# Kernel optimization log

Measured on AMD Instinct MI355X. Metric: run time of the kernel, lower is better.

The kernel has to match this reference:

```python
import jax, jax.numpy as jnp
import numpy as np

N_CLASSES = 4
N_STEPS = 10
THRESHOLD = 0.7
ALPHA = 2.0


def _make_kernel_bias(n_classes, threshold):
    cross = np.zeros((3, 3, 3), dtype=np.float32)
    cross[1, 1, :] = 1.0
    cross[1, :, 1] = 1.0
    cross[:, 1, 1] = 1.0
    # depthwise kernel, OIDHW with I = 1 (groups = n_classes)
    kernel = (1.0 / 7.0 / (1.0 - threshold)) * np.tile(cross[None, None], (n_classes, 1, 1, 1, 1))
    bias = np.full((n_classes,), -threshold / (1.0 - threshold), dtype=np.float32)
    return jnp.asarray(kernel), jnp.asarray(bias)


def setup_inputs() -> dict:
    key = jax.random.key(0)
    k1, k2, k3 = jax.random.split(key, 3)
    B, C, D, H, W = 2, N_CLASSES, 128, 128, 128
    inp = jax.random.normal(k1, (B, C, D, H, W), dtype=jnp.float32)
    target = jax.random.randint(k2, (B, D, H, W), 0, C, dtype=jnp.int64)
    weight = jax.random.uniform(k3, (B, C), dtype=jnp.float32)
    kernel, bias = _make_kernel_bias(C, THRESHOLD)
    return {"input": inp, "target": target, "weight": weight, "kernel": kernel, "bias": bias}


def _erode(op, kernel, bias, n_classes):
    y = jax.lax.conv_general_dilated(
        op, kernel, window_strides=(1, 1, 1), padding=[(1, 1)] * 3,
        dimension_numbers=("NCDHW", "OIDHW", "NCDHW"),
        feature_group_count=n_classes)
    return jnp.maximum(y + bias[None, :, None, None, None], 0.0)


def reference(input, target, weight, kernel, bias):
    C = N_CLASSES
    probs = jax.nn.softmax(input, axis=1)
    # one_hot -> [B, D, H, W, C] -> [B, C, D, H, W]
    tgt = jnp.transpose(jax.nn.one_hot(target, C, dtype=probs.dtype), (0, 4, 1, 2, 3))
    op = jnp.square(probs - tgt)
    loss_t = jnp.zeros_like(op)
    for k in range(N_STEPS):
        op = _erode(op, kernel, bias, C)
        loss_t = loss_t + (float(k + 1) ** ALPHA) * op
    loss_t = loss_t * weight[:, :, None, None, None]
    return jnp.mean(loss_t)
```

## Files before the change

kernel.cpp:

```cpp
#include <hip/hip_runtime.h>

#define DHW   (128*128*128)
#define CDHW  (4*DHW)
#define NTOT  (2*CDHW)
#define NACC  1024

#define ROW4     32
#define IN_ROWS  12
#define S1_ROWS  10
#define IN_P4    (IN_ROWS*ROW4)
#define S1_P4    (S1_ROWS*ROW4)
#define SLOT4(z) (((z)+8)&3)
#define SLOT2(z) (((z)+8)&1)


__global__ __launch_bounds__(256, 4) void fused_sm_erode2_kernel(
    const float* __restrict__ in, const int* __restrict__ tgt,
    float4* __restrict__ dst,
    const float* __restrict__ kern, const float* __restrict__ bias,
    const float* __restrict__ weight, float c1, float c2,
    double* __restrict__ accs, int* __restrict__ flagOut)
{
    __shared__ float4 lin[4 * IN_P4];
    __shared__ float4 ls1[2 * S1_P4];
    __shared__ double wsum[4];
    __shared__ int    voteArr[16];

    const int tid = threadIdx.x;
    const int x  = blockIdx.x & 7;
    const int q  = blockIdx.x >> 3;
    const int c  = q & 3;
    const int t  = x * 32 + (q >> 2);
    const int y0 = (t & 15) << 3;
    const int zb = ((t >> 4) & 7) << 4;
    const int b  = (t >> 7) & 1;
    const int bc = b * 4 + c;
    const int fid = (bc << 7) | (((t >> 4) & 7) << 4) | (t & 15);

    const float4* in4 = (const float4*)in;
    const int4*   tg4 = (const int4*)tgt;
    const size_t  chb = ((size_t)(b * 4)) << 19;
    const size_t  co0 = chb + ((size_t)c << 19);
    const size_t  co1 = chb + ((size_t)((c + 1) & 3) << 19);
    const size_t  co2 = chb + ((size_t)((c + 2) & 3) << 19);
    const size_t  co3 = chb + ((size_t)((c + 3) & 3) << 19);
    float4*       dp  = dst + ((size_t)bc << 19);
    const float wk = kern[13];
    const float bs = bias[c];

    const int col  = tid & 31;
    const int trow = tid >> 5;

    if (tid < 16) voteArr[tid] = 0;

    const int  gy0  = y0 + trow - 2;
    const bool lv0  = ((unsigned)gy0 < 128u);
    const int  off0 = (lv0 ? gy0 : 0) * 32 + col;
    const bool act1 = (tid < 128);
    const int  gy1  = y0 + trow + 6;
    const bool lv1  = act1 && ((unsigned)gy1 < 128u);
    const int  off1 = (lv1 ? gy1 : 0) * 32 + col;

    const bool  sact1 = (tid < 64);
    const int   sr  = (tid < 32) ? 0 : 9;
    const float m1  = ((unsigned)(y0 + sr - 1) < 128u) ? 1.f : 0.f;
    const int   ci1 = (sr + 1) * 32 + (tid & 31);
    const int   so1 = sr * 32 + (tid & 31);

    const float lmask = (col == 0)  ? 0.f : 1.f;
    const float rmask = (col == 31) ? 0.f : 1.f;

    const int go4 = (y0 + trow) * 32 + col;

    const float4 f4z = make_float4(0.f, 0.f, 0.f, 0.f);
    float4 A00 = f4z, A01 = f4z, A02 = f4z, A03 = f4z;
    float4 A10 = f4z, A11 = f4z, A12 = f4z, A13 = f4z;
    int4   T0 = make_int4(0,0,0,0), T1 = make_int4(0,0,0,0);
    bool   ok0 = false, ok1 = false;
    float4 s_m = f4z, s_c = f4z, s_p = f4z;
    float4 vH  = f4z;

    auto prefetch = [&](int L) {
        const bool zok = ((unsigned)L < 128u);
        ok0 = zok && lv0;
        ok1 = zok && lv1;
        if (ok0) {
            size_t o = (size_t)(L << 12) + off0;
            A00 = in4[co0 + o];
            A01 = in4[co1 + o];
            A02 = in4[co2 + o];
            A03 = in4[co3 + o];
            T0  = tg4[((size_t)b << 19) + o];
        }
        if (ok1) {
            size_t o = (size_t)(L << 12) + off1;
            A10 = in4[co0 + o];
            A11 = in4[co1 + o];
            A12 = in4[co2 + o];
            A13 = in4[co3 + o];
            T1  = tg4[((size_t)b << 19) + o];
        }
    };
    auto op_one = [&](const float4& B0, const float4& B1, const float4& B2,
                      const float4& B3, const int4& T) -> float4 {
        float4 r;
        #define OP1(K)                                                         \
        {                                                                      \
            float vc = B0.K;                                                   \
            float sm = 1.0f + __expf(B1.K - vc) + __expf(B2.K - vc)            \
                            + __expf(B3.K - vc);                               \
            float d  = __builtin_amdgcn_rcpf(sm) - ((T.K == c) ? 1.0f : 0.0f); \
            r.K = d * d;                                                       \
        }
        OP1(x) OP1(y) OP1(z) OP1(w)
        #undef OP1
        return r;
    };
    auto commit = [&](int L) {
        float4* sl = lin + SLOT4(L) * IN_P4;
        float4 v0 = f4z, v1 = f4z;
        if (ok0) v0 = op_one(A00, A01, A02, A03, T0);
        if (ok1) v1 = op_one(A10, A11, A12, A13, T1);
        sl[tid] = v0;
        if (act1) sl[256 + tid] = v1;
    };
    auto s1one = [&](const float4* pzm, const float4* pzc, const float4* pzp,
                     int ci, float ym) -> float4 {
        float4 qC = pzc[ci];
        float4 qU = pzc[ci - 32];
        float4 qD = pzc[ci + 32];
        float4 qm = pzm[ci];
        float4 qp = pzp[ci];
        float lf = __shfl_up(qC.w, 1, 64)   * lmask;
        float rt = __shfl_down(qC.x, 1, 64) * rmask;
        float4 v;
        v.x = fmaxf((qC.x + lf   + qC.y + qU.x + qD.x + qm.x + qp.x) * wk + bs, 0.f) * ym;
        v.y = fmaxf((qC.y + qC.x + qC.z + qU.y + qD.y + qm.y + qp.y) * wk + bs, 0.f) * ym;
        v.z = fmaxf((qC.z + qC.y + qC.w + qU.z + qD.z + qm.z + qp.z) * wk + bs, 0.f) * ym;
        v.w = fmaxf((qC.w + qC.z + rt   + qU.w + qD.w + qm.w + qp.w) * wk + bs, 0.f) * ym;
        return v;
    };
    auto s1_phase = [&](int z) {
        float4* o = ls1 + SLOT2(z) * S1_P4;
        float4 vnew;
        if ((unsigned)z < 128u) {
            const float4* pzm = lin + SLOT4(z - 1) * IN_P4;
            const float4* pzc = lin + SLOT4(z)     * IN_P4;
            const float4* pzp = lin + SLOT4(z + 1) * IN_P4;
            vnew = s1one(pzm, pzc, pzp, tid + 64, 1.f);
            o[tid + 32] = vnew;
            if (sact1) o[so1] = s1one(pzm, pzc, pzp, ci1, m1);
        } else {
            vnew = f4z;
            o[tid + 32] = f4z;
            if (sact1) o[so1] = f4z;
        }
        s_m = s_c; s_c = s_p; s_p = vnew;
    };

    double part = 0.0;

    prefetch(zb - 2); commit(zb - 2);
    prefetch(zb - 1); commit(zb - 1);
    prefetch(zb);     commit(zb);
    prefetch(zb + 1);
    __syncthreads();
    s1_phase(zb - 1);

    for (int L = zb + 1; L <= zb + 17; ++L) {
        commit(L);
        __syncthreads();
        const int zp = L - 3;
        if (zp >= zb && voteArr[zp - zb] != 0)
            dp[((size_t)zp << 12) + go4] = vH;
        if (L <= zb + 16) prefetch(L + 1);
        s1_phase(L - 1);
        const int zo = L - 2;
        if (zo >= zb) {
            const float4* su = ls1 + SLOT2(zo) * S1_P4;
            float4 u4 = su[tid];
            float4 d4 = su[tid + 64];
            float lf = __shfl_up(s_c.w, 1, 64)   * lmask;
            float rt = __shfl_down(s_c.x, 1, 64) * rmask;
            float4 v;
            v.x = fmaxf((s_c.x + lf    + s_c.y + u4.x + d4.x + s_m.x + s_p.x) * wk + bs, 0.f);
            v.y = fmaxf((s_c.y + s_c.x + s_c.z + u4.y + d4.y + s_m.y + s_p.y) * wk + bs, 0.f);
            v.z = fmaxf((s_c.z + s_c.y + s_c.w + u4.z + d4.z + s_m.z + s_p.z) * wk + bs, 0.f);
            v.w = fmaxf((s_c.w + s_c.z + rt    + u4.w + d4.w + s_m.w + s_p.w) * wk + bs, 0.f);
            float pl = c1 * (s_c.x + s_c.y + s_c.z + s_c.w)
                     + c2 * (v.x   + v.y   + v.z   + v.w);
            part += (double)pl;
            bool nzv = (v.x != 0.f) || (v.y != 0.f) || (v.z != 0.f) || (v.w != 0.f);
            if (__any(nzv) && (tid & 63) == 0) atomicOr(&voteArr[zo - zb], 1);
            vH = v;
        }
    }

    __syncthreads();
    if (voteArr[15] != 0) dp[((size_t)(zb + 15) << 12) + go4] = vH;

    #pragma unroll
    for (int off = 32; off > 0; off >>= 1)
        part += __shfl_down(part, off, 64);
    if ((tid & 63) == 0) wsum[tid >> 6] = part;
    __syncthreads();
    if (tid == 0) {
        int mask = 0;
        #pragma unroll
        for (int i = 0; i < 16; ++i) mask |= (voteArr[i] ? 1 : 0) << i;
        flagOut[fid] = mask;
        double tot = (wsum[0] + wsum[1] + wsum[2] + wsum[3]) * (double)weight[bc];
        accs[blockIdx.x] = tot;
    }
}

__global__ __launch_bounds__(256, 4) void erode2_kernel(
    const float4* __restrict__ src, float4* __restrict__ dst,
    const float* __restrict__ kern, const float* __restrict__ bias,
    const float* __restrict__ weight, float c1, float c2,
    int store, double* __restrict__ accs,
    const int* __restrict__ flagIn, int* __restrict__ flagOut)
{
    __shared__ float4 lin[4 * IN_P4];
    __shared__ float4 ls1[2 * S1_P4];
    __shared__ double wsum[4];
    __shared__ int    sf[9];
    __shared__ int    voteArr[16];

    const int tid = threadIdx.x;
    const int bid = ((blockIdx.x & 7) << 7) | (blockIdx.x >> 3);
    const int ty = bid & 15;
    const int tz = (bid >> 4) & 7;
    const int y0 = ty << 3;
    const int zb = tz << 4;
    const int bc = bid >> 7;

    if (tid < 9) {
        int dy = tid % 3 - 1, dz = tid / 3 - 1;
        int yt = ty + dy, zt = tz + dz;
        int f = 0;
        if ((unsigned)yt < 16u && (unsigned)zt < 8u)
            f = flagIn[(bc << 7) | (zt << 4) | yt];
        sf[tid] = f;
    }
    if (tid < 16) voteArr[tid] = 0;
    __syncthreads();

    unsigned aInW = 0;
    #pragma unroll
    for (int i = 0; i < 20; ++i) {
        int L = zb - 2 + i;
        if ((unsigned)L < 128u) {
            int zi = (L >> 4) - tz + 1;
            int m  = sf[zi * 3] | sf[zi * 3 + 1] | sf[zi * 3 + 2];
            aInW |= (unsigned)((m >> (L & 15)) & 1) << i;
        }
    }
    if (aInW == 0) {
        if (tid == 0) flagOut[bid] = 0;
        return;
    }
    const unsigned aS1W = aInW | (aInW << 1) | (aInW >> 1);
    const unsigned aS2W = aS1W | (aS1W << 1) | (aS1W >> 1);

    const float4* sp = src + ((size_t)bc << 19);
    float4*       dp = dst + ((size_t)bc << 19);
    const float wk = kern[13];
    const float bs = bias[bc & 3];

    const int col  = tid & 31;
    const int trow = tid >> 5;

    const int  gy0  = y0 + trow - 2;
    const bool lv0  = ((unsigned)gy0 < 128u);
    const int  off0 = (lv0 ? gy0 : 0) * 32 + col;
    const bool act1 = (tid < 128);
    const int  gy1  = y0 + trow + 6;
    const bool lv1  = act1 && ((unsigned)gy1 < 128u);
    const int  off1 = (lv1 ? gy1 : 0) * 32 + col;

    const int yd0c = (unsigned)((gy0 >> 3) - ty + 1) < 3u ? ((gy0 >> 3) - ty + 1) : 1;
    const int yd1c = (unsigned)((gy1 >> 3) - ty + 1) < 3u ? ((gy1 >> 3) - ty + 1) : 1;

    const bool  sact1 = (tid < 64);
    const int   sr  = (tid < 32) ? 0 : 9;
    const float m1  = ((unsigned)(y0 + sr - 1) < 128u) ? 1.f : 0.f;
    const int   ci1 = (sr + 1) * 32 + (tid & 31);
    const int   so1 = sr * 32 + (tid & 31);

    const float lmask = (col == 0)  ? 0.f : 1.f;
    const float rmask = (col == 31) ? 0.f : 1.f;

    const int go4 = (y0 + trow) * 32 + col;

    const float4 f4z = make_float4(0.f, 0.f, 0.f, 0.f);
    float4 pf0 = f4z, pf1 = f4z;
    float4 s_m = f4z, s_c = f4z, s_p = f4z;
    float4 vH  = f4z;

    auto prefetch = [&](int L) {
        pf0 = f4z; pf1 = f4z;
        if ((unsigned)L < 128u) {
            const int zi = (L >> 4) - tz + 1;
            const int sh = L & 15;
            const float4* zp = sp + ((size_t)L << 12);
            if (lv0 && ((sf[zi * 3 + yd0c] >> sh) & 1)) pf0 = zp[off0];
            if (lv1 && ((sf[zi * 3 + yd1c] >> sh) & 1)) pf1 = zp[off1];
        }
    };
    auto commit = [&](int L) {
        float4* sl = lin + SLOT4(L) * IN_P4;
        sl[tid] = pf0;
        if (act1) sl[256 + tid] = pf1;
    };
    auto s1one = [&](const float4* pzm, const float4* pzc, const float4* pzp,
                     int ci, float ym) -> float4 {
        float4 qC = pzc[ci];
        float4 qU = pzc[ci - 32];
        float4 qD = pzc[ci + 32];
        float4 qm = pzm[ci];
        float4 qp = pzp[ci];
        float lf = __shfl_up(qC.w, 1, 64)   * lmask;
        float rt = __shfl_down(qC.x, 1, 64) * rmask;
        float4 v;
        v.x = fmaxf((qC.x + lf   + qC.y + qU.x + qD.x + qm.x + qp.x) * wk + bs, 0.f) * ym;
        v.y = fmaxf((qC.y + qC.x + qC.z + qU.y + qD.y + qm.y + qp.y) * wk + bs, 0.f) * ym;
        v.z = fmaxf((qC.z + qC.y + qC.w + qU.z + qD.z + qm.z + qp.z) * wk + bs, 0.f) * ym;
        v.w = fmaxf((qC.w + qC.z + rt   + qU.w + qD.w + qm.w + qp.w) * wk + bs, 0.f) * ym;
        return v;
    };
    auto s1_phase = [&](int z) {
        float4 vnew = f4z;
        if ((unsigned)z < 128u && ((aS1W >> (z - zb + 2)) & 1)) {
            float4* o = ls1 + SLOT2(z) * S1_P4;
            const float4* pzm = lin + SLOT4(z - 1) * IN_P4;
            const float4* pzc = lin + SLOT4(z)     * IN_P4;
            const float4* pzp = lin + SLOT4(z + 1) * IN_P4;
            vnew = s1one(pzm, pzc, pzp, tid + 64, 1.f);
            o[tid + 32] = vnew;
            if (sact1) o[so1] = s1one(pzm, pzc, pzp, ci1, m1);
        }
        s_m = s_c; s_c = s_p; s_p = vnew;
    };

    double part = 0.0;

    prefetch(zb - 2); commit(zb - 2);
    prefetch(zb - 1); commit(zb - 1);
    prefetch(zb);     commit(zb);
    prefetch(zb + 1);
    __syncthreads();
    s1_phase(zb - 1);

    for (int L = zb + 1; L <= zb + 17; ++L) {
        commit(L);
        __syncthreads();
        const int zp = L - 3;
        if (store && zp >= zb && voteArr[zp - zb] != 0)
            dp[((size_t)zp << 12) + go4] = vH;
        if (L <= zb + 16) prefetch(L + 1);
        s1_phase(L - 1);
        const int zo = L - 2;
        if (zo >= zb) {
            float4 v = f4z;
            if ((aS2W >> (zo - zb + 2)) & 1) {
                float4 u4 = f4z, d4 = f4z;
                if ((aS1W >> (zo - zb + 2)) & 1) {
                    const float4* su = ls1 + SLOT2(zo) * S1_P4;
                    u4 = su[tid];
                    d4 = su[tid + 64];
                }
                float lf = __shfl_up(s_c.w, 1, 64)   * lmask;
                float rt = __shfl_down(s_c.x, 1, 64) * rmask;
                v.x = fmaxf((s_c.x + lf    + s_c.y + u4.x + d4.x + s_m.x + s_p.x) * wk + bs, 0.f);
                v.y = fmaxf((s_c.y + s_c.x + s_c.z + u4.y + d4.y + s_m.y + s_p.y) * wk + bs, 0.f);
                v.z = fmaxf((s_c.z + s_c.y + s_c.w + u4.z + d4.z + s_m.z + s_p.z) * wk + bs, 0.f);
                v.w = fmaxf((s_c.w + s_c.z + rt    + u4.w + d4.w + s_m.w + s_p.w) * wk + bs, 0.f);
                float pl = c1 * (s_c.x + s_c.y + s_c.z + s_c.w)
                         + c2 * (v.x   + v.y   + v.z   + v.w);
                part += (double)pl;
                bool nzv = (v.x != 0.f) || (v.y != 0.f) || (v.z != 0.f) || (v.w != 0.f);
                if (__any(nzv) && (tid & 63) == 0) atomicOr(&voteArr[zo - zb], 1);
            }
            vH = v;
        }
    }

    __syncthreads();
    if (store && voteArr[15] != 0) dp[((size_t)(zb + 15) << 12) + go4] = vH;

    #pragma unroll
    for (int off = 32; off > 0; off >>= 1)
        part += __shfl_down(part, off, 64);
    if ((tid & 63) == 0) wsum[tid >> 6] = part;
    __syncthreads();
    if (tid == 0) {
        int mask = 0;
        #pragma unroll
        for (int i = 0; i < 16; ++i) mask |= (voteArr[i] ? 1 : 0) << i;
        flagOut[bid] = mask;
        double tot = (wsum[0] + wsum[1] + wsum[2] + wsum[3]) * (double)weight[bc];
        atomicAdd(&accs[bid], tot);
    }
}

__global__ __launch_bounds__(1024) void finalize_kernel(
    const double* __restrict__ accs, float* __restrict__ out)
{
    __shared__ double wsum[16];
    double v = accs[threadIdx.x];
    #pragma unroll
    for (int off = 32; off > 0; off >>= 1)
        v += __shfl_down(v, off, 64);
    int lane = threadIdx.x & 63;
    int wid  = threadIdx.x >> 6;
    if (lane == 0) wsum[wid] = v;
    __syncthreads();
    if (threadIdx.x == 0) {
        double tot = 0.0;
        #pragma unroll
        for (int i = 0; i < 16; ++i) tot += wsum[i];
        out[0] = (float)(tot / (double)NTOT);
    }
}

extern "C" void kernel_launch(void* const* d_in, const int* in_sizes, int n_in,
                              void* d_out, int out_size, void* d_ws, size_t ws_size,
                              hipStream_t stream) {
    const float* in     = (const float*)d_in[0];
    const int*   tgt    = (const int*)d_in[1];
    const float* weight = (const float*)d_in[2];
    const float* kern   = (const float*)d_in[3];
    const float* bias   = (const float*)d_in[4];
    float* out = (float*)d_out;

    char* ws = (char*)d_ws;
    float*  buf0   = (float*)ws;
    float*  buf1   = (float*)(ws + (size_t)NTOT * sizeof(float));
    double* accs   = (double*)(ws + (size_t)NTOT * 2 * sizeof(float));
    int*    flagsA = (int*)(ws + (size_t)NTOT * 2 * sizeof(float) + NACC * sizeof(double));
    int*    flagsB = flagsA + NACC;

    fused_sm_erode2_kernel<<<1024, 256, 0, stream>>>(
        in, tgt, (float4*)buf0, kern, bias, weight, 1.0f, 4.0f, accs, flagsA);

    float* cur = buf0;
    float* nxt = buf1;
    int*   fIn = flagsA;
    int*   fOut = flagsB;
    for (int p = 1; p < 5; ++p) {
        float c1 = (float)((2 * p + 1) * (2 * p + 1));
        float c2 = (float)((2 * p + 2) * (2 * p + 2));
        int   store = (p < 4) ? 1 : 0;
        erode2_kernel<<<1024, 256, 0, stream>>>(
            (const float4*)cur, (float4*)nxt, kern, bias, weight, c1, c2,
            store, accs, fIn, fOut);
        float* tb = cur; cur = nxt; nxt = tb;
        int*   tf = fIn; fIn = fOut; fOut = tf;
    }

    finalize_kernel<<<1, 1024, 0, stream>>>(accs, out);
}
```

Before: 155.3 us.

## Fuse four erosion steps per kernel pass to halve intermediate passes

```diff
diff --git a/kernel.cpp b/kernel.cpp
--- a/kernel.cpp
+++ b/kernel.cpp
@@ -214,15 +214,23 @@
     }
 }
 
-__global__ __launch_bounds__(256, 4) void erode2_kernel(
+#define E4_INP4  512
+#define E4_S1P4  448
+#define E4_S2P4  384
+#define E4_S3P4  320
+
+__global__ __launch_bounds__(256, 2) void erode4_kernel(
     const float4* __restrict__ src, float4* __restrict__ dst,
     const float* __restrict__ kern, const float* __restrict__ bias,
-    const float* __restrict__ weight, float c1, float c2,
+    const float* __restrict__ weight,
+    float c1, float c2, float c3, float c4,
     int store, double* __restrict__ accs,
     const int* __restrict__ flagIn, int* __restrict__ flagOut)
 {
-    __shared__ float4 lin[4 * IN_P4];
-    __shared__ float4 ls1[2 * S1_P4];
+    __shared__ float4 lin[4 * E4_INP4];
+    __shared__ float4 ls1[2 * E4_S1P4];
+    __shared__ float4 ls2[2 * E4_S2P4];
+    __shared__ float4 ls3[2 * E4_S3P4];
     __shared__ double wsum[4];
     __shared__ int    sf[9];
     __shared__ int    voteArr[16];
@@ -246,22 +254,23 @@
     if (tid < 16) voteArr[tid] = 0;
     __syncthreads();
 
-    unsigned aInW = 0;
+    unsigned aIn = 0, zc = 0;
     #pragma unroll
-    for (int i = 0; i < 20; ++i) {
-        int L = zb - 2 + i;
+    for (int i = 0; i < 24; ++i) {
+        int L = zb - 4 + i;
         if ((unsigned)L < 128u) {
+            zc |= 1u << i;
             int zi = (L >> 4) - tz + 1;
-            int m  = sf[zi * 3] | sf[zi * 3 + 1] | sf[zi * 3 + 2];
-            aInW |= (unsigned)((m >> (L & 15)) & 1) << i;
-        }
-    }
-    if (aInW == 0) {
-        if (tid == 0) flagOut[bid] = 0;
-        return;
-    }
-    const unsigned aS1W = aInW | (aInW << 1) | (aInW >> 1);
-    const unsigned aS2W = aS1W | (aS1W << 1) | (aS1W >> 1);
+            int m = sf[zi * 3] | sf[zi * 3 + 1] | sf[zi * 3 + 2];
+            aIn |= (unsigned)((m >> (L & 15)) & 1) << i;
+        }
+    }
+    if (aIn == 0) { if (tid == 0) flagOut[bid] = 0; return; }
+
+    const unsigned a1 = (aIn | aIn << 1 | aIn >> 1) & zc & 0x7FFFFEu;
+    const unsigned a2 = (a1  | a1  << 1 | a1  >> 1) & zc & 0x3FFFFCu;
+    const unsigned a3 = (a2  | a2  << 1 | a2  >> 1) & zc & 0x1FFFF8u;
+    const unsigned a4 = (a3  | a3  << 1 | a3  >> 1) & zc & 0x0FFFF0u;
 
     const float4* sp = src + ((size_t)bc << 19);
     float4*       dp = dst + ((size_t)bc << 19);
@@ -270,117 +279,161 @@
 
     const int col  = tid & 31;
     const int trow = tid >> 5;
-
-    const int  gy0  = y0 + trow - 2;
-    const bool lv0  = ((unsigned)gy0 < 128u);
+    const int g    = trow;
+
+    const int  gy0 = y0 - 4 + trow;
+    const int  gy1 = y0 + 4 + trow;
+    const bool lv0 = ((unsigned)gy0 < 128u);
+    const bool lv1 = ((unsigned)gy1 < 128u);
     const int  off0 = (lv0 ? gy0 : 0) * 32 + col;
-    const bool act1 = (tid < 128);
-    const int  gy1  = y0 + trow + 6;
-    const bool lv1  = act1 && ((unsigned)gy1 < 128u);
     const int  off1 = (lv1 ? gy1 : 0) * 32 + col;
-
-    const int yd0c = (unsigned)((gy0 >> 3) - ty + 1) < 3u ? ((gy0 >> 3) - ty + 1) : 1;
-    const int yd1c = (unsigned)((gy1 >> 3) - ty + 1) < 3u ? ((gy1 >> 3) - ty + 1) : 1;
-
-    const bool  sact1 = (tid < 64);
-    const int   sr  = (tid < 32) ? 0 : 9;
-    const float m1  = ((unsigned)(y0 + sr - 1) < 128u) ? 1.f : 0.f;
-    const int   ci1 = (sr + 1) * 32 + (tid & 31);
-    const int   so1 = sr * 32 + (tid & 31);
+    const int  yd0 = ((unsigned)((gy0 >> 3) - ty + 1) < 3u) ? ((gy0 >> 3) - ty + 1) : 1;
+    const int  yd1 = ((unsigned)((gy1 >> 3) - ty + 1) < 3u) ? ((gy1 >> 3) - ty + 1) : 1;
+
+    const int   r1  = (g < 3) ? g : g + 8;
+    const float ym1 = ((unsigned)(y0 - 3 + r1) < 128u) ? 1.f : 0.f;
+    const int   ci1 = (r1 + 1) * 32 + col;
+    const int   R2  = (g < 2) ? g : g + 8;
+    const float ym2 = ((unsigned)(y0 - 2 + R2) < 128u) ? 1.f : 0.f;
+    const int   ci2 = (R2 + 2) * 32 + col;
+    const int   S3  = g * 9;
+    const float ym3 = ((unsigned)(y0 - 1 + S3) < 128u) ? 1.f : 0.f;
+    const int   ci3 = (S3 + 3) * 32 + col;
 
     const float lmask = (col == 0)  ? 0.f : 1.f;
     const float rmask = (col == 31) ? 0.f : 1.f;
-
-    const int go4 = (y0 + trow) * 32 + col;
+    const int   go4  = (y0 + trow) * 32 + col;
 
     const float4 f4z = make_float4(0.f, 0.f, 0.f, 0.f);
     float4 pf0 = f4z, pf1 = f4z;
-    float4 s_m = f4z, s_c = f4z, s_p = f4z;
-    float4 vH  = f4z;
-
+    float4 p1m=f4z,p1c=f4z,p1p=f4z;
+    float4 p2m=f4z,p2c=f4z,p2p=f4z;
+    float4 p3m=f4z,p3c=f4z,p3p=f4z;
+    float4 o1m=f4z,o1c=f4z,o1p=f4z;
+    float4 q1m=f4z,q1c=f4z,q1p=f4z;
+    float4 q2m=f4z,q2c=f4z,q2p=f4z;
+    float4 vH = f4z;
+    double part = 0.0;
+
+    auto st7 = [&](const float4& zm, const float4& cc, const float4& zp,
+                   const float4& u, const float4& d, float ym) -> float4 {
+        float lf = __shfl_up(cc.w, 1, 64)   * lmask;
+        float rt = __shfl_down(cc.x, 1, 64) * rmask;
+        float4 v;
+        v.x = fmaxf((cc.x + lf   + cc.y + u.x + d.x + zm.x + zp.x) * wk + bs, 0.f) * ym;
+        v.y = fmaxf((cc.y + cc.x + cc.z + u.y + d.y + zm.y + zp.y) * wk + bs, 0.f) * ym;
+        v.z = fmaxf((cc.z + cc.y + cc.w + u.z + d.z + zm.z + zp.z) * wk + bs, 0.f) * ym;
+        v.w = fmaxf((cc.w + cc.z + rt   + u.w + d.w + zm.w + zp.w) * wk + bs, 0.f) * ym;
+        return v;
+    };
+    auto s1at = [&](int z, int ci, float ym) -> float4 {
+        const float4* pzm = lin + SLOT4(z - 1) * E4_INP4;
+        const float4* pzc = lin + SLOT4(z)     * E4_INP4;
+        const float4* pzp = lin + SLOT4(z + 1) * E4_INP4;
+        return st7(pzm[ci], pzc[ci], pzp[ci], pzc[ci - 32], pzc[ci + 32], ym);
+    };
     auto prefetch = [&](int L) {
         pf0 = f4z; pf1 = f4z;
-        if ((unsigned)L < 128u) {
+        if (L >= zb - 4 && L <= zb + 19 && (unsigned)L < 128u) {
             const int zi = (L >> 4) - tz + 1;
             const int sh = L & 15;
             const float4* zp = sp + ((size_t)L << 12);
-            if (lv0 && ((sf[zi * 3 + yd0c] >> sh) & 1)) pf0 = zp[off0];
-            if (lv1 && ((sf[zi * 3 + yd1c] >> sh) & 1)) pf1 = zp[off1];
+            if (lv0 && ((sf[zi * 3 + yd0] >> sh) & 1)) pf0 = zp[off0];
+            if (lv1 && ((sf[zi * 3 + yd1] >> sh) & 1)) pf1 = zp[off1];
         }
     };
     auto commit = [&](int L) {
-        float4* sl = lin + SLOT4(L) * IN_P4;
-        sl[tid] = pf0;
-        if (act1) sl[256 + tid] = pf1;
-    };
-    auto s1one = [&](const float4* pzm, const float4* pzc, const float4* pzp,
-                     int ci, float ym) -> float4 {
-        float4 qC = pzc[ci];
-        float4 qU = pzc[ci - 32];
-        float4 qD = pzc[ci + 32];
-        float4 qm = pzm[ci];
-        float4 qp = pzp[ci];
-        float lf = __shfl_up(qC.w, 1, 64)   * lmask;
-        float rt = __shfl_down(qC.x, 1, 64) * rmask;
-        float4 v;
-        v.x = fmaxf((qC.x + lf   + qC.y + qU.x + qD.x + qm.x + qp.x) * wk + bs, 0.f) * ym;
-        v.y = fmaxf((qC.y + qC.x + qC.z + qU.y + qD.y + qm.y + qp.y) * wk + bs, 0.f) * ym;
-        v.z = fmaxf((qC.z + qC.y + qC.w + qU.z + qD.z + qm.z + qp.z) * wk + bs, 0.f) * ym;
-        v.w = fmaxf((qC.w + qC.z + rt   + qU.w + qD.w + qm.w + qp.w) * wk + bs, 0.f) * ym;
-        return v;
-    };
-    auto s1_phase = [&](int z) {
-        float4 vnew = f4z;
-        if ((unsigned)z < 128u && ((aS1W >> (z - zb + 2)) & 1)) {
-            float4* o = ls1 + SLOT2(z) * S1_P4;
-            const float4* pzm = lin + SLOT4(z - 1) * IN_P4;
-            const float4* pzc = lin + SLOT4(z)     * IN_P4;
-            const float4* pzp = lin + SLOT4(z + 1) * IN_P4;
-            vnew = s1one(pzm, pzc, pzp, tid + 64, 1.f);
-            o[tid + 32] = vnew;
-            if (sact1) o[so1] = s1one(pzm, pzc, pzp, ci1, m1);
-        }
-        s_m = s_c; s_c = s_p; s_p = vnew;
-    };
-
-    double part = 0.0;
-
-    prefetch(zb - 2); commit(zb - 2);
-    prefetch(zb - 1); commit(zb - 1);
-    prefetch(zb);     commit(zb);
-    prefetch(zb + 1);
-    __syncthreads();
-    s1_phase(zb - 1);
-
-    for (int L = zb + 1; L <= zb + 17; ++L) {
+        float4* sl = lin + SLOT4(L) * E4_INP4;
+        sl[trow * 32 + col]       = pf0;
+        sl[(trow + 8) * 32 + col] = pf1;
+    };
+
+    prefetch(zb - 4);
+    for (int L = zb - 4; L <= zb + 19; ++L) {
         commit(L);
         __syncthreads();
-        const int zp = L - 3;
-        if (store && zp >= zb && voteArr[zp - zb] != 0)
-            dp[((size_t)zp << 12) + go4] = vH;
-        if (L <= zb + 16) prefetch(L + 1);
-        s1_phase(L - 1);
-        const int zo = L - 2;
-        if (zo >= zb) {
+        const int zs = L - 5;
+        if (store && zs >= zb && voteArr[zs - zb] != 0)
+            dp[((size_t)zs << 12) + go4] = vH;
+        if (L < zb + 19) prefetch(L + 1);
+
+        {
+            const int z = L - 1, ib = z - (zb - 4);
+            float4 vp = f4z, vo = f4z, vq = f4z;
+            if ((unsigned)ib < 24u && ((a1 >> ib) & 1)) {
+                vp = s1at(z, (trow + 4) * 32 + col, 1.f);
+                float4* o = ls1 + SLOT2(z) * E4_S1P4;
+                if (tid < 192) o[r1 * 32 + col] = s1at(z, ci1, ym1);
+                if (tid < 128) vo = s1at(z, ci2, ym2);
+                if (tid < 64)  vq = s1at(z, ci3, ym3);
+                o[(trow + 3) * 32 + col] = vp;
+                if (z >= zb && z <= zb + 15)
+                    part += (double)(c1 * (vp.x + vp.y + vp.z + vp.w));
+            }
+            p1m = p1c; p1c = p1p; p1p = vp;
+            o1m = o1c; o1c = o1p; o1p = vo;
+            q1m = q1c; q1c = q1p; q1p = vq;
+        }
+        {
+            const int z = L - 2, ib = z - (zb - 4);
+            float4 vp = f4z, vq = f4z;
+            if ((unsigned)ib < 24u && ((a2 >> ib) & 1)) {
+                const bool l1 = ((a1 >> ib) & 1);
+                const float4* s1p_ = ls1 + SLOT2(z) * E4_S1P4;
+                float4 u = l1 ? s1p_[(trow + 2) * 32 + col] : f4z;
+                float4 d = l1 ? s1p_[(trow + 4) * 32 + col] : f4z;
+                vp = st7(p1m, p1c, p1p, u, d, 1.f);
+                float4* o = ls2 + SLOT2(z) * E4_S2P4;
+                if (tid < 128) {
+                    float4 u2 = l1 ? s1p_[R2 * 32 + col]       : f4z;
+                    float4 d2 = l1 ? s1p_[(R2 + 2) * 32 + col] : f4z;
+                    o[R2 * 32 + col] = st7(o1m, o1c, o1p, u2, d2, ym2);
+                }
+                if (tid < 64) {
+                    float4 u3 = l1 ? s1p_[(S3 + 1) * 32 + col] : f4z;
+                    float4 d3 = l1 ? s1p_[(S3 + 3) * 32 + col] : f4z;
+                    vq = st7(q1m, q1c, q1p, u3, d3, ym3);
+                }
+                o[(trow + 2) * 32 + col] = vp;
+                if (z >= zb && z <= zb + 15)
+                    part += (double)(c2 * (vp.x + vp.y + vp.z + vp.w));
+            }
+            p2m = p2c; p2c = p2p; p2p = vp;
+            q2m = q2c; q2c = q2p; q2p = vq;
+        }
+        {
+            const int z = L - 3, ib = z - (zb - 4);
+            float4 vp = f4z;
+            if ((unsigned)ib < 24u && ((a3 >> ib) & 1)) {
+                const bool l2 = ((a2 >> ib) & 1);
+                const float4* s2p_ = ls2 + SLOT2(z) * E4_S2P4;
+                float4 u = l2 ? s2p_[(trow + 1) * 32 + col] : f4z;
+                float4 d = l2 ? s2p_[(trow + 3) * 32 + col] : f4z;
+                vp = st7(p2m, p2c, p2p, u, d, 1.f);
+                float4* o = ls3 + SLOT2(z) * E4_S3P4;
+                if (tid < 64) {
+                    float4 u3 = l2 ? s2p_[S3 * 32 + col]       : f4z;
+                    float4 d3 = l2 ? s2p_[(S3 + 2) * 32 + col] : f4z;
+                    o[S3 * 32 + col] = st7(q2m, q2c, q2p, u3, d3, ym3);
+                }
+                o[(trow + 1) * 32 + col] = vp;
+                if (z >= zb && z <= zb + 15)
+                    part += (double)(c3 * (vp.x + vp.y + vp.z + vp.w));
+            }
+            p3m = p3c; p3c = p3p; p3p = vp;
+        }
+        {
+            const int z = L - 4, ib = z - (zb - 4);
             float4 v = f4z;
-            if ((aS2W >> (zo - zb + 2)) & 1) {
-                float4 u4 = f4z, d4 = f4z;
-                if ((aS1W >> (zo - zb + 2)) & 1) {
-                    const float4* su = ls1 + SLOT2(zo) * S1_P4;
-                    u4 = su[tid];
-                    d4 = su[tid + 64];
-                }
-                float lf = __shfl_up(s_c.w, 1, 64)   * lmask;
-                float rt = __shfl_down(s_c.x, 1, 64) * rmask;
-                v.x = fmaxf((s_c.x + lf    + s_c.y + u4.x + d4.x + s_m.x + s_p.x) * wk + bs, 0.f);
-                v.y = fmaxf((s_c.y + s_c.x + s_c.z + u4.y + d4.y + s_m.y + s_p.y) * wk + bs, 0.f);
-                v.z = fmaxf((s_c.z + s_c.y + s_c.w + u4.z + d4.z + s_m.z + s_p.z) * wk + bs, 0.f);
-                v.w = fmaxf((s_c.w + s_c.z + rt    + u4.w + d4.w + s_m.w + s_p.w) * wk + bs, 0.f);
-                float pl = c1 * (s_c.x + s_c.y + s_c.z + s_c.w)
-                         + c2 * (v.x   + v.y   + v.z   + v.w);
-                part += (double)pl;
+            if ((unsigned)ib < 24u && ((a4 >> ib) & 1)) {
+                const bool l3 = ((a3 >> ib) & 1);
+                const float4* s3p_ = ls3 + SLOT2(z) * E4_S3P4;
+                float4 u = l3 ? s3p_[trow * 32 + col]       : f4z;
+                float4 d = l3 ? s3p_[(trow + 2) * 32 + col] : f4z;
+                v = st7(p3m, p3c, p3p, u, d, 1.f);
+                part += (double)(c4 * (v.x + v.y + v.z + v.w));
                 bool nzv = (v.x != 0.f) || (v.y != 0.f) || (v.z != 0.f) || (v.w != 0.f);
-                if (__any(nzv) && (tid & 63) == 0) atomicOr(&voteArr[zo - zb], 1);
+                if (__any(nzv) && (tid & 63) == 0) atomicOr(&voteArr[z - zb], 1);
             }
             vH = v;
         }
@@ -444,20 +497,13 @@
     fused_sm_erode2_kernel<<<1024, 256, 0, stream>>>(
         in, tgt, (float4*)buf0, kern, bias, weight, 1.0f, 4.0f, accs, flagsA);
 
-    float* cur = buf0;
-    float* nxt = buf1;
-    int*   fIn = flagsA;
-    int*   fOut = flagsB;
-    for (int p = 1; p < 5; ++p) {
-        float c1 = (float)((2 * p + 1) * (2 * p + 1));
-        float c2 = (float)((2 * p + 2) * (2 * p + 2));
-        int   store = (p < 4) ? 1 : 0;
-        erode2_kernel<<<1024, 256, 0, stream>>>(
-            (const float4*)cur, (float4*)nxt, kern, bias, weight, c1, c2,
-            store, accs, fIn, fOut);
-        float* tb = cur; cur = nxt; nxt = tb;
-        int*   tf = fIn; fIn = fOut; fOut = tf;
-    }
+    erode4_kernel<<<1024, 256, 0, stream>>>(
+        (const float4*)buf0, (float4*)buf1, kern, bias, weight,
+        9.0f, 16.0f, 25.0f, 36.0f, 1, accs, flagsA, flagsB);
+
+    erode4_kernel<<<1024, 256, 0, stream>>>(
+        (const float4*)buf1, (float4*)buf0, kern, bias, weight,
+        49.0f, 64.0f, 81.0f, 100.0f, 0, accs, flagsB, flagsA);
 
     finalize_kernel<<<1, 1024, 0, stream>>>(accs, out);
 }
```

Result: no change. 153.9 us (-0.9%).
